# Optimization experiments

Measured on AMD Instinct MI355X. Metric: run time of the kernel, lower is better.

The kernel has to match this reference:

```python
import jax, jax.numpy as jnp
import numpy as np

B = 8192      # env batch
M = 16        # n_machine
HID = 128     # machine_hidden_dim
HEADS = 1
BN_EPS = 1e-5


def _gat(h, gat_W, gat_a):
    # h: (B2, 2, HID); gat_W: (HID, HEADS*HID); gat_a: (HEADS, 2*HID, 1)
    B2 = h.shape[0]
    Wh = (h @ gat_W).reshape(B2, 2, HEADS, HID).transpose(0, 2, 1, 3)  # (B2,H,2,hid)
    src = jnp.einsum('bhnf,hfo->bhno', Wh, gat_a[:, :HID, :])   # (B2,H,2,1)
    tgt = jnp.einsum('bhnf,hfo->bhno', Wh, gat_a[:, HID:, :])   # (B2,H,2,1)
    e = jax.nn.leaky_relu(src + jnp.swapaxes(tgt, -1, -2), negative_slope=0.2)  # (B2,H,2,2)
    # static adjacency: row0 attends to both nodes, row1 only to itself (2->1 directed)
    adj = jnp.array([[1.0, 1.0], [0.0, 1.0]], dtype=e.dtype)
    e = jnp.where(adj > 0, e, jnp.asarray(-9e15, e.dtype))
    att = jax.nn.softmax(e, axis=-1)
    h_prime = att @ Wh                 # (B2,H,2,hid)
    return h_prime.mean(axis=1)        # concat=False -> mean over heads -> (B2,2,hid)


def setup_inputs() -> dict:
    key = jax.random.key(0)
    ks = jax.random.split(key, 24)
    s = 0.05
    inp = {
        'machine_fea_1': jax.random.normal(ks[0], (B, M, 6), jnp.float32),
        'machine_fea_2': jax.random.normal(ks[1], (B, M, 8), jnp.float32),
        'h_pooled_o': jax.random.normal(ks[2], (B, HID), jnp.float32),
        'machine_mask': jnp.zeros((B, 1, M), dtype=bool),
        # params (Linear weights stored as (in, out); original Linears have bias=False for feature projections)
        'W1': jax.random.normal(ks[3], (6, HID), jnp.float32) * s,
        'W2': jax.random.normal(ks[4], (8, HID), jnp.float32) * s,
        'gat_W': jax.random.normal(ks[5], (HID, HEADS * HID), jnp.float32) * s,
        'gat_a': jax.random.normal(ks[6], (HEADS, 2 * HID, 1), jnp.float32) * s,
        'bn_gamma': jnp.ones((HID,), jnp.float32),
        'bn_beta': jnp.zeros((HID,), jnp.float32),
        # MLPActor: 3 layers, in=3*HID, hidden=HID, out=1 (tanh hidden, linear out)
        'Wa1': jax.random.normal(ks[7], (3 * HID, HID), jnp.float32) * s,
        'ba1': jnp.zeros((HID,), jnp.float32),
        'Wa2': jax.random.normal(ks[8], (HID, HID), jnp.float32) * s,
        'ba2': jnp.zeros((HID,), jnp.float32),
        'Wa3': jax.random.normal(ks[9], (HID, 1), jnp.float32) * s,
        'ba3': jnp.zeros((1,), jnp.float32),
        # MLPCritic: 3 layers, in=HID, hidden=HID, out=2
        'Wc1': jax.random.normal(ks[10], (HID, HID), jnp.float32) * s,
        'bc1': jnp.zeros((HID,), jnp.float32),
        'Wc2': jax.random.normal(ks[11], (HID, HID), jnp.float32) * s,
        'bc2': jnp.zeros((HID,), jnp.float32),
        'Wc3': jax.random.normal(ks[12], (HID, 2), jnp.float32) * s,
        'bc3': jnp.zeros((2,), jnp.float32),
    }
    return inp


def reference(machine_fea_1, machine_fea_2, h_pooled_o, machine_mask,
              W1, W2, gat_W, gat_a, bn_gamma, bn_beta,
              Wa1, ba1, Wa2, ba2, Wa3, ba3,
              Wc1, bc1, Wc2, bc2, Wc3, bc3):
    m_fea1 = machine_fea_1 @ W1                       # (B,M,HID)
    m_fea2 = machine_fea_2 @ W2                       # (B,M,HID)
    # pair the two projections per machine node: (B*M, 2, HID)
    h12 = jnp.stack([m_fea1.reshape(-1, HID), m_fea2.reshape(-1, HID)], axis=1)
    g = jax.nn.elu(_gat(h12, gat_W, gat_a))
    g = jax.nn.elu(_gat(g, gat_W, gat_a))
    g = _gat(g, gat_W, gat_a)
    # NOTE: h_machine_feas is computed but unused downstream in the original forward (ablation)
    h_machine_feas = g.mean(axis=-2).reshape(-1, M, HID)
    # BatchNorm1d in training mode over flattened (B*M, HID)
    flat = m_fea1.reshape(-1, HID)
    mu = flat.mean(axis=0)
    var = flat.var(axis=0)  # biased, as torch BN uses for normalization
    h_m_nodes = (((flat - mu) / jnp.sqrt(var + BN_EPS)) * bn_gamma + bn_beta).reshape(-1, M, HID)
    h_pooled = h_m_nodes.mean(axis=1)                 # (B,HID)
    concat = jnp.concatenate([
        h_m_nodes,
        jnp.broadcast_to(h_pooled[:, None, :], h_m_nodes.shape),
        jnp.broadcast_to(h_pooled_o[:, None, :], h_m_nodes.shape),
    ], axis=-1)                                       # (B,M,3*HID)
    x = jnp.tanh(concat @ Wa1 + ba1)
    x = jnp.tanh(x @ Wa2 + ba2)
    mch_scores = (x @ Wa3 + ba3).squeeze(-1) * 10.0   # (B,M)
    mask = machine_mask.squeeze(1)
    mch_scores = jnp.where(mask, -jnp.inf, mch_scores)
    mch_prob = jax.nn.softmax(mch_scores, axis=-1)
    v = jnp.tanh(h_pooled @ Wc1 + bc1)
    v = jnp.tanh(v @ Wc2 + bc2)
    machine_v = v @ Wc3 + bc3                         # (B,2)
    return (mch_prob, h_pooled, machine_v)
```

## Files before the change

kernel.cpp:

```cpp
#include <hip/hip_runtime.h>
#include <hip/hip_bf16.h>
#include <math.h>

#define HID    128
#define BATCH  8192
#define NM     16
#define NROWS  (BATCH * NM)
#define BN_EPS 1e-5f

#define S1_BLOCKS   256
#define S1_ROWS     (NROWS / S1_BLOCKS)
#define PREP_BLOCKS 32
#define TOT_BLOCKS  (S1_BLOCKS + PREP_BLOCKS)

#define WS_PART  0
#define WS_SCALE 8192
#define WS_SHIFT 8320
#define WS_M1    8448
#define WS_SV    9216
#define WS_N1    9344
#define WS_CV    10112
#define WS_BW    10240

#define O1 ((size_t)BATCH * NM)
#define O2 (O1 + (size_t)BATCH * HID)

#define G    4
#define ROWS (G * NM)
#define LDH  136
#define ZLD  136
#define LDV  132
#define HLD  24

typedef __attribute__((ext_vector_type(8))) short short8_t;
typedef __attribute__((ext_vector_type(4))) float f32x4;

#define MFMA16(a, b, c) __builtin_amdgcn_mfma_f32_16x16x32_bf16(a, b, c, 0, 0, 0)

__device__ __forceinline__ unsigned short f2bf(float x) {
    __hip_bfloat16 h = __float2bfloat16(x);
    return *reinterpret_cast<unsigned short*>(&h);
}
__device__ __forceinline__ float bf2f(unsigned short u) {
    __hip_bfloat16 h = *reinterpret_cast<__hip_bfloat16*>(&u);
    return __bfloat162float(h);
}
__device__ __forceinline__ float ftanh(float x) {
    float e = __expf(2.0f * x);
    return 1.0f - 2.0f / (e + 1.0f);
}

__global__ __launch_bounds__(512) void stats_prep_kernel(
    const float* __restrict__ fea1,
    const float* __restrict__ Wa1, const float* __restrict__ Wa2,
    const float* __restrict__ Wc2,
    float* __restrict__ ws, unsigned short* __restrict__ wbt)
{
    const int tid = threadIdx.x;
    const int blk = blockIdx.x;

    if (blk >= S1_BLOCKS) {
        const int idx = (blk - S1_BLOCKS) * 512 + tid;
        const int k = idx >> 7, c = idx & 127;
        wbt[c * 128 + k]         = f2bf(Wa1[idx]);
        wbt[16384 + c * 128 + k] = f2bf(Wa2[idx]);
        wbt[32768 + c * 128 + k] = f2bf(Wa1[32768 + idx]);
        wbt[49152 + c * 128 + k] = f2bf(Wc2[idx]);
        return;
    }

    __shared__ float feaS[S1_ROWS * 6];
    __shared__ float redM[8 * 27];

    const float* src = fea1 + (size_t)blk * (S1_ROWS * 6);
    for (int i = tid; i < S1_ROWS * 6; i += 512) feaS[i] = src[i];
    __syncthreads();

    float f[6];
    #pragma unroll
    for (int j = 0; j < 6; ++j) f[j] = feaS[tid * 6 + j];

    float acc[27];
    #pragma unroll
    for (int j = 0; j < 6; ++j) acc[j] = f[j];
    {
        int idx = 6;
        #pragma unroll
        for (int j = 0; j < 6; ++j)
            #pragma unroll
            for (int k = j; k < 6; ++k) acc[idx++] = f[j] * f[k];
    }
    #pragma unroll
    for (int j = 0; j < 27; ++j) {
        acc[j] += __shfl_xor(acc[j], 1);
        acc[j] += __shfl_xor(acc[j], 2);
        acc[j] += __shfl_xor(acc[j], 4);
        acc[j] += __shfl_xor(acc[j], 8);
        acc[j] += __shfl_xor(acc[j], 16);
        acc[j] += __shfl_xor(acc[j], 32);
    }
    const int wv = tid >> 6;
    if ((tid & 63) == 0) {
        #pragma unroll
        for (int j = 0; j < 27; ++j) redM[wv * 27 + j] = acc[j];
    }
    __syncthreads();
    if (tid < 27) {
        float s = 0.f;
        #pragma unroll
        for (int w2 = 0; w2 < 8; ++w2) s += redM[w2 * 27 + tid];
        ws[WS_PART + blk * 32 + tid] = s;
    }
}

__global__ __launch_bounds__(512) void finalize_kernel(
    const float* __restrict__ W1,  const float* __restrict__ Wa1,
    const float* __restrict__ Wc1, const float* __restrict__ bc1,
    const float* __restrict__ gamma, const float* __restrict__ beta,
    float* __restrict__ ws, unsigned short* __restrict__ wbt)
{
    __shared__ double momS[27];
    __shared__ float scS2[HID], shS[HID];
    __shared__ float w1sS[6 * HID];
    __shared__ float partS[4 * 7 * HID];

    const int tid = threadIdx.x;
    const int blk = blockIdx.x;

    {
        const int j = tid >> 4;
        const int l = tid & 15;
        double s = 0.0;
        if (j < 27)
            for (int p = l; p < S1_BLOCKS; p += 16)
                s += (double)ws[WS_PART + p * 32 + j];
        s += __shfl_xor(s, 1);
        s += __shfl_xor(s, 2);
        s += __shfl_xor(s, 4);
        s += __shfl_xor(s, 8);
        if (j < 27 && l == 0) momS[j] = s;
    }
    __syncthreads();

    if (tid < 128) {
        float wv[6];
        #pragma unroll
        for (int j = 0; j < 6; ++j) wv[j] = W1[j * HID + tid];
        double sum = 0.0, ssq = 0.0;
        #pragma unroll
        for (int j = 0; j < 6; ++j) sum += (double)wv[j] * momS[j];
        {
            int idx = 6;
            #pragma unroll
            for (int j = 0; j < 6; ++j)
                #pragma unroll
                for (int k = j; k < 6; ++k) {
                    double t = (double)wv[j] * (double)wv[k] * momS[idx++];
                    ssq += (j == k) ? t : 2.0 * t;
                }
        }
        const double inv = 1.0 / (double)NROWS;
        double mu  = sum * inv;
        double var = ssq * inv - mu * mu;
        float sc = gamma[tid] * rsqrtf((float)var + BN_EPS);
        float sh = beta[tid] - (float)mu * sc;
        scS2[tid] = sc;
        shS[tid]  = sh;
        if (blk == 0) {
            ws[WS_SCALE + tid] = sc;
            ws[WS_SHIFT + tid] = sh;
        }
    }
    __syncthreads();
    for (int i = tid; i < 6 * HID; i += 512)
        w1sS[i] = W1[i] * scS2[i & 127];
    __syncthreads();

    if (blk == 2) {
        for (int idx = tid; idx < HID * 32; idx += 512) {
            const int col = idx >> 5, k = idx & 31;
            unsigned short v = 0;
            int kr = -1; bool lo = false;
            if (k < 6)                    kr = k;
            else if (k >= 8  && k < 14)   kr = k - 8;
            else if (k >= 16 && k < 22) { kr = k - 16; lo = true; }
            if (kr >= 0) {
                const float wv = w1sS[kr * HID + col];
                const unsigned short hi = f2bf(wv);
                v = lo ? f2bf(wv - bf2f(hi)) : hi;
            }
            wbt[65536 + col * 32 + k] = v;
        }
        return;
    }

    {
        const float* st = (blk == 0) ? (Wa1 + 16384) : Wc1;
        const int cc = tid & 127;
        const int kq = tid >> 7;
        float a[7] = {0.f, 0.f, 0.f, 0.f, 0.f, 0.f, 0.f};
        for (int k = kq * 32; k < kq * 32 + 32; ++k) {
            const float sv = st[k * 128 + cc];
            #pragma unroll
            for (int j = 0; j < 6; ++j)
                a[j] += w1sS[j * HID + k] * sv;
            a[6] += shS[k] * sv;
        }
        #pragma unroll
        for (int j = 0; j < 7; ++j)
            partS[(kq * 7 + j) * HID + cc] = a[j];
    }
    __syncthreads();
    if (tid < 128) {
        #pragma unroll
        for (int j = 0; j < 7; ++j) {
            const float v = partS[(0 * 7 + j) * HID + tid]
                          + partS[(1 * 7 + j) * HID + tid]
                          + partS[(2 * 7 + j) * HID + tid]
                          + partS[(3 * 7 + j) * HID + tid];
            if (blk == 0) {
                if (j < 6) ws[WS_M1 + j * HID + tid] = v;
                else       ws[WS_SV + tid] = v;
            } else {
                if (j < 6) ws[WS_N1 + j * HID + tid] = v;
                else       ws[WS_CV + tid] = v + bc1[tid];
            }
        }
    }
}

__global__ __launch_bounds__(256, 4) void main_kernel(
    const float* __restrict__ fea1, const float* __restrict__ hpo,
    const unsigned char* __restrict__ mask,
    const float* __restrict__ W1,
    const float* __restrict__ ba1, const float* __restrict__ ba2,
    const float* __restrict__ Wa3, const float* __restrict__ ba3,
    const float* __restrict__ bc2,
    const float* __restrict__ Wc3, const float* __restrict__ bc3,
    const float* __restrict__ ws, const unsigned short* __restrict__ wbt,
    float* __restrict__ out)
{
    __shared__ __align__(16) unsigned short hmS[ROWS * LDH];
    __shared__ __align__(16) unsigned short x1S[ROWS * LDH];
    __shared__ __align__(16) unsigned short zS[G * ZLD];
    __shared__ __align__(16) unsigned short v1bS[4 * LDV];
    __shared__ __align__(16) unsigned short v2bS[4 * LDV];
    __shared__ float scS[4 * ROWS];
    __shared__ float fmS[4][8];

    float* feaS = (float*)x1S;
    unsigned short* feaHL = x1S + 768;

    const int tid = threadIdx.x;
    const int b0  = blockIdx.x * G;

    const int w    = tid >> 6;
    const int lane = tid & 63;
    const int lr   = lane & 15;
    const int lg   = lane >> 4;
    const int n0   = 2 * w;

    const unsigned short* wbt1  = wbt;
    const unsigned short* wbt2  = wbt + 16384;
    const unsigned short* wbtB  = wbt + 32768;
    const unsigned short* wbtC2 = wbt + 49152;
    const unsigned short* wbtW1 = wbt + 65536;

    for (int i = tid; i < ROWS * 6; i += 256) {
        const float x = fea1[(size_t)b0 * (NM * 6) + i];
        feaS[i] = x;
        const int r = i / 6, j = i - r * 6;
        const unsigned short hx = f2bf(x);
        const unsigned short lx = f2bf(x - bf2f(hx));
        feaHL[r * HLD + j]     = hx;
        feaHL[r * HLD + 8 + j] = lx;
    }
    if (tid < 64) {
        feaHL[tid * HLD + 6]  = 0;
        feaHL[tid * HLD + 7]  = 0;
        feaHL[tid * HLD + 14] = 0;
        feaHL[tid * HLD + 15] = 0;
    } else if (tid < 80) {
        feaHL[64 * HLD + (tid - 64)] = 0;
    }
    for (int i = tid; i < G * HID; i += 256) {
        const int g = i >> 7, cc = i & 127;
        zS[g * ZLD + cc] = f2bf(hpo[(size_t)b0 * HID + i]);
    }

    short8_t bW[2];
    #pragma unroll
    for (int t = 0; t < 2; ++t)
        bW[t] = *(const short8_t*)(wbtW1 + ((n0 + t) * 16 + lr) * 32 + lg * 8);
    short8_t b1f[2][4];
    #pragma unroll
    for (int t = 0; t < 2; ++t) {
        const unsigned short* br = wbt1 + ((n0 + t) * 16 + lr) * 128 + lg * 8;
        #pragma unroll
        for (int kk = 0; kk < 4; ++kk) b1f[t][kk] = *(const short8_t*)(br + kk * 32);
    }
    const float sh0 = ws[WS_SHIFT + n0 * 16 + lr];
    const float sh1 = ws[WS_SHIFT + (n0 + 1) * 16 + lr];
    __syncthreads();

    const int hloff = (lg == 1) ? 8 : 0;
    #pragma unroll
    for (int g = 0; g < 4; ++g) {
        const int row = (lg == 3) ? 64 : (g * 16 + lr);
        short8_t af = *(const short8_t*)(feaHL + row * HLD + hloff);

        #pragma unroll
        for (int t = 0; t < 2; ++t) {
            const float sh = t ? sh1 : sh0;
            f32x4 acc = {sh, sh, sh, sh};
            acc = MFMA16(af, bW[t], acc);
            #pragma unroll
            for (int i = 0; i < 4; ++i)
                hmS[(g * 16 + lg * 4 + i) * LDH + (n0 + t) * 16 + lr] = f2bf(acc[i]);
        }
    }
    if (tid < 24) {
        const int g = tid / 6, j = tid % 6;
        float s = 0.f;
        for (int m = 0; m < NM; ++m) s += feaS[(g * 16 + m) * 6 + j];
        fmS[g][j] = s * (1.0f / NM);
    }
    __syncthreads();

    f32x4 accB[2];
    {
        short8_t bBf[2][4];
        #pragma unroll
        for (int t = 0; t < 2; ++t) {
            const unsigned short* br = wbtB + ((n0 + t) * 16 + lr) * 128 + lg * 8;
            #pragma unroll
            for (int kk = 0; kk < 4; ++kk) bBf[t][kk] = *(const short8_t*)(br + kk * 32);
        }
        short8_t za[4];
        const unsigned short* zr = zS + (lr & 3) * ZLD + lg * 8;
        #pragma unroll
        for (int kk = 0; kk < 4; ++kk) za[kk] = *(const short8_t*)(zr + kk * 32);

        float fm[4][6];
        #pragma unroll
        for (int g = 0; g < 4; ++g)
            #pragma unroll
            for (int j = 0; j < 6; ++j) fm[g][j] = fmS[g][j];

        #pragma unroll
        for (int t = 0; t < 2; ++t) {
            const int col = (n0 + t) * 16 + lr;
            const float bias = ba1[col] + ws[WS_SV + col];
            float b_[4];
            #pragma unroll
            for (int g = 0; g < 4; ++g) {
                float a = bias;
                #pragma unroll
                for (int j = 0; j < 6; ++j) a += fm[g][j] * ws[WS_M1 + j * HID + col];
                b_[g] = a;
            }
            f32x4 acc = {b_[0], b_[1], b_[2], b_[3]};
            acc = MFMA16(za[0], bBf[t][0], acc);
            acc = MFMA16(za[1], bBf[t][1], acc);
            acc = MFMA16(za[2], bBf[t][2], acc);
            acc = MFMA16(za[3], bBf[t][3], acc);
            accB[t] = acc;
        }

        #pragma unroll
        for (int t = 0; t < 2; ++t) {
            const int col = (n0 + t) * 16 + lr;
            float a = ws[WS_CV + col];
            #pragma unroll
            for (int j = 0; j < 6; ++j) a += fm[lg][j] * ws[WS_N1 + j * HID + col];
            v1bS[lg * LDV + col] = f2bf(ftanh(a));
        }

        #pragma unroll
        for (int t = 0; t < 2; ++t) {
            const int col = (n0 + t) * 16 + lr;
            float a = 0.f;
            #pragma unroll
            for (int j = 0; j < 6; ++j) a += fm[lg][j] * W1[j * HID + col];
            a = a * ws[WS_SCALE + col] + ws[WS_SHIFT + col];
            out[O1 + (size_t)(b0 + lg) * HID + col] = a;
        }
    }

    short8_t b2f[2][4];
    #pragma unroll
    for (int t = 0; t < 2; ++t) {
        const unsigned short* br = wbt2 + ((n0 + t) * 16 + lr) * 128 + lg * 8;
        #pragma unroll
        for (int kk = 0; kk < 4; ++kk) b2f[t][kk] = *(const short8_t*)(br + kk * 32);
    }

    #pragma unroll
    for (int g = 0; g < 4; ++g) {
        short8_t ha[4];
        const unsigned short* ar = hmS + (g * 16 + lr) * LDH + lg * 8;
        #pragma unroll
        for (int kk = 0; kk < 4; ++kk) ha[kk] = *(const short8_t*)(ar + kk * 32);
        #pragma unroll
        for (int t = 0; t < 2; ++t) {
            const float bz = accB[t][g];
            f32x4 acc = {bz, bz, bz, bz};
            acc = MFMA16(ha[0], b1f[t][0], acc);
            acc = MFMA16(ha[1], b1f[t][1], acc);
            acc = MFMA16(ha[2], b1f[t][2], acc);
            acc = MFMA16(ha[3], b1f[t][3], acc);
            #pragma unroll
            for (int i = 0; i < 4; ++i)
                x1S[(g * 16 + lg * 4 + i) * LDH + (n0 + t) * 16 + lr] = f2bf(ftanh(acc[i]));
        }
    }
    __syncthreads();

    {
        short8_t va[4];
        const unsigned short* vr = v1bS + (lr & 3) * LDV + lg * 8;
        #pragma unroll
        for (int kk = 0; kk < 4; ++kk) va[kk] = *(const short8_t*)(vr + kk * 32);
        #pragma unroll
        for (int t = 0; t < 2; ++t) {
            const int n = n0 + t;
            const unsigned short* br = wbtC2 + (n * 16 + lr) * 128 + lg * 8;
            const float bi = bc2[n * 16 + lr];
            f32x4 acc = {bi, bi, bi, bi};
            acc = MFMA16(va[0], *(const short8_t*)(br),      acc);
            acc = MFMA16(va[1], *(const short8_t*)(br + 32), acc);
            acc = MFMA16(va[2], *(const short8_t*)(br + 64), acc);
            acc = MFMA16(va[3], *(const short8_t*)(br + 96), acc);
            if (lg == 0) {
                #pragma unroll
                for (int i = 0; i < 4; ++i)
                    v2bS[i * LDV + n * 16 + lr] = f2bf(ftanh(acc[i]));
            }
        }

        float p[4][4];
        #pragma unroll
        for (int g = 0; g < 4; ++g)
            #pragma unroll
            for (int i = 0; i < 4; ++i) p[g][i] = 0.f;

        const float wv0 = Wa3[n0 * 16 + lr];
        const float wv1 = Wa3[(n0 + 1) * 16 + lr];
        const float bi0 = ba2[n0 * 16 + lr];
        const float bi1 = ba2[(n0 + 1) * 16 + lr];
        #pragma unroll
        for (int g = 0; g < 4; ++g) {
            short8_t ha[4];
            const unsigned short* ar = x1S + (g * 16 + lr) * LDH + lg * 8;
            #pragma unroll
            for (int kk = 0; kk < 4; ++kk) ha[kk] = *(const short8_t*)(ar + kk * 32);
            #pragma unroll
            for (int t = 0; t < 2; ++t) {
                const float bi = t ? bi1 : bi0;
                f32x4 acc = {bi, bi, bi, bi};
                acc = MFMA16(ha[0], b2f[t][0], acc);
                acc = MFMA16(ha[1], b2f[t][1], acc);
                acc = MFMA16(ha[2], b2f[t][2], acc);
                acc = MFMA16(ha[3], b2f[t][3], acc);
                const float wv = t ? wv1 : wv0;
                #pragma unroll
                for (int i = 0; i < 4; ++i)
                    p[g][i] += ftanh(acc[i]) * wv;
            }
        }
        #pragma unroll
        for (int g = 0; g < 4; ++g) {
            #pragma unroll
            for (int i = 0; i < 4; ++i) {
                float v = p[g][i];
                v += __shfl_xor(v, 1);
                v += __shfl_xor(v, 2);
                v += __shfl_xor(v, 4);
                v += __shfl_xor(v, 8);
                if (lr == 0) scS[w * ROWS + g * 16 + lg * 4 + i] = v;
            }
        }
    }
    __syncthreads();

    {
        const int g = w;
        float s = scS[0 * ROWS + g * 16 + lr] + scS[1 * ROWS + g * 16 + lr]
                + scS[2 * ROWS + g * 16 + lr] + scS[3 * ROWS + g * 16 + lr];
        s = (s + ba3[0]) * 10.0f;
        if (mask[(size_t)(b0 + g) * NM + lr]) s = -INFINITY;
        float mx = s;
        mx = fmaxf(mx, __shfl_xor(mx, 1));
        mx = fmaxf(mx, __shfl_xor(mx, 2));
        mx = fmaxf(mx, __shfl_xor(mx, 4));
        mx = fmaxf(mx, __shfl_xor(mx, 8));
        float e = __expf(s - mx);
        float sum = e;
        sum += __shfl_xor(sum, 1);
        sum += __shfl_xor(sum, 2);
        sum += __shfl_xor(sum, 4);
        sum += __shfl_xor(sum, 8);
        if (lane < NM)
            out[(size_t)(b0 + g) * NM + lr] = e / sum;
    }

    {
        const int g = w;
        const int k2 = lane * 2;
        float v0 = bf2f(v2bS[g * LDV + k2]);
        float v1 = bf2f(v2bS[g * LDV + k2 + 1]);
        float4 wc = *(const float4*)(Wc3 + k2 * 2);
        float p0 = v0 * wc.x + v1 * wc.z;
        float p1 = v0 * wc.y + v1 * wc.w;
        p0 += __shfl_xor(p0, 1);  p1 += __shfl_xor(p1, 1);
        p0 += __shfl_xor(p0, 2);  p1 += __shfl_xor(p1, 2);
        p0 += __shfl_xor(p0, 4);  p1 += __shfl_xor(p1, 4);
        p0 += __shfl_xor(p0, 8);  p1 += __shfl_xor(p1, 8);
        p0 += __shfl_xor(p0, 16); p1 += __shfl_xor(p1, 16);
        p0 += __shfl_xor(p0, 32); p1 += __shfl_xor(p1, 32);
        if (lane == 0) {
            out[O2 + (size_t)(b0 + g) * 2 + 0] = p0 + bc3[0];
            out[O2 + (size_t)(b0 + g) * 2 + 1] = p1 + bc3[1];
        }
    }
}

extern "C" void kernel_launch(void* const* d_in, const int* in_sizes, int n_in,
                              void* d_out, int out_size, void* d_ws, size_t ws_size,
                              hipStream_t stream)
{
    const float* fea1  = (const float*)d_in[0];
    const float* hpo   = (const float*)d_in[2];
    const unsigned char* mask = (const unsigned char*)d_in[3];
    const float* W1    = (const float*)d_in[4];
    const float* gamma = (const float*)d_in[8];
    const float* beta  = (const float*)d_in[9];
    const float* Wa1   = (const float*)d_in[10];
    const float* ba1   = (const float*)d_in[11];
    const float* Wa2   = (const float*)d_in[12];
    const float* ba2   = (const float*)d_in[13];
    const float* Wa3   = (const float*)d_in[14];
    const float* ba3   = (const float*)d_in[15];
    const float* Wc1   = (const float*)d_in[16];
    const float* bc1   = (const float*)d_in[17];
    const float* Wc2   = (const float*)d_in[18];
    const float* bc2   = (const float*)d_in[19];
    const float* Wc3   = (const float*)d_in[20];
    const float* bc3   = (const float*)d_in[21];

    float* ws = (float*)d_ws;
    unsigned short* wbt = (unsigned short*)(ws + WS_BW);
    float* out = (float*)d_out;

    stats_prep_kernel<<<TOT_BLOCKS, 512, 0, stream>>>(
        fea1, Wa1, Wa2, Wc2, ws, wbt);
    finalize_kernel<<<3, 512, 0, stream>>>(
        W1, Wa1, Wc1, bc1, gamma, beta, ws, wbt);
    main_kernel<<<BATCH / G, 256, 0, stream>>>(
        fea1, hpo, mask, W1, ba1, ba2, Wa3, ba3,
        bc2, Wc3, bc3, ws, wbt, out);
}
```

Baseline: 67.62 us.

## Double batch tile per block and give each wave one 16-column slice

The main kernel now handles 8 batch elements per block with 512 threads (8 waves) instead of 4 elements with 4 waves. Each wave owns one 16-column output slice instead of two, so it holds half as many weight fragments in registers, and each weight fragment is reused across 8 row groups. The z-projection MFMA outputs are shared between lane groups with cross-lane shuffles, and the score reduction now sums over 8 per-wave partials. This halves the grid size and doubles LDS use per block, which may lower occupancy or leave fewer blocks to balance across CUs.

```diff
diff --git a/kernel.cpp b/kernel.cpp
--- a/kernel.cpp
+++ b/kernel.cpp
@@ -25,7 +25,7 @@
 #define O1 ((size_t)BATCH * NM)
 #define O2 (O1 + (size_t)BATCH * HID)
 
-#define G    4
+#define G    8
 #define ROWS (G * NM)
 #define LDH  136
 #define ZLD  136
@@ -229,7 +229,7 @@
     }
 }
 
-__global__ __launch_bounds__(256, 4) void main_kernel(
+__global__ __launch_bounds__(512, 4) void main_kernel(
     const float* __restrict__ fea1, const float* __restrict__ hpo,
     const unsigned char* __restrict__ mask,
     const float* __restrict__ W1,
@@ -243,13 +243,13 @@
     __shared__ __align__(16) unsigned short hmS[ROWS * LDH];
     __shared__ __align__(16) unsigned short x1S[ROWS * LDH];
     __shared__ __align__(16) unsigned short zS[G * ZLD];
-    __shared__ __align__(16) unsigned short v1bS[4 * LDV];
-    __shared__ __align__(16) unsigned short v2bS[4 * LDV];
-    __shared__ float scS[4 * ROWS];
-    __shared__ float fmS[4][8];
+    __shared__ __align__(16) unsigned short v1bS[G * LDV];
+    __shared__ __align__(16) unsigned short v2bS[G * LDV];
+    __shared__ float scS[8 * ROWS];
+    __shared__ float fmS[G][8];
 
     float* feaS = (float*)x1S;
-    unsigned short* feaHL = x1S + 768;
+    unsigned short* feaHL = x1S + 1536;
 
     const int tid = threadIdx.x;
     const int b0  = blockIdx.x * G;
@@ -258,7 +258,7 @@
     const int lane = tid & 63;
     const int lr   = lane & 15;
     const int lg   = lane >> 4;
-    const int n0   = 2 * w;
+    const int col  = w * 16 + lr;
 
     const unsigned short* wbt1  = wbt;
     const unsigned short* wbt2  = wbt + 16384;
@@ -266,7 +266,7 @@
     const unsigned short* wbtC2 = wbt + 49152;
     const unsigned short* wbtW1 = wbt + 65536;
 
-    for (int i = tid; i < ROWS * 6; i += 256) {
+    for (int i = tid; i < ROWS * 6; i += 512) {
         const float x = fea1[(size_t)b0 * (NM * 6) + i];
         feaS[i] = x;
         const int r = i / 6, j = i - r * 6;
@@ -275,51 +275,41 @@
         feaHL[r * HLD + j]     = hx;
         feaHL[r * HLD + 8 + j] = lx;
     }
-    if (tid < 64) {
+    if (tid < ROWS) {
         feaHL[tid * HLD + 6]  = 0;
         feaHL[tid * HLD + 7]  = 0;
         feaHL[tid * HLD + 14] = 0;
         feaHL[tid * HLD + 15] = 0;
-    } else if (tid < 80) {
-        feaHL[64 * HLD + (tid - 64)] = 0;
-    }
-    for (int i = tid; i < G * HID; i += 256) {
+    } else if (tid < ROWS + 16) {
+        feaHL[ROWS * HLD + (tid - ROWS)] = 0;
+    }
+    for (int i = tid; i < G * HID; i += 512) {
         const int g = i >> 7, cc = i & 127;
         zS[g * ZLD + cc] = f2bf(hpo[(size_t)b0 * HID + i]);
     }
 
-    short8_t bW[2];
-    #pragma unroll
-    for (int t = 0; t < 2; ++t)
-        bW[t] = *(const short8_t*)(wbtW1 + ((n0 + t) * 16 + lr) * 32 + lg * 8);
-    short8_t b1f[2][4];
-    #pragma unroll
-    for (int t = 0; t < 2; ++t) {
-        const unsigned short* br = wbt1 + ((n0 + t) * 16 + lr) * 128 + lg * 8;
-        #pragma unroll
-        for (int kk = 0; kk < 4; ++kk) b1f[t][kk] = *(const short8_t*)(br + kk * 32);
-    }
-    const float sh0 = ws[WS_SHIFT + n0 * 16 + lr];
-    const float sh1 = ws[WS_SHIFT + (n0 + 1) * 16 + lr];
+    short8_t bW = *(const short8_t*)(wbtW1 + col * 32 + lg * 8);
+    short8_t b1f[4];
+    {
+        const unsigned short* br = wbt1 + col * 128 + lg * 8;
+        #pragma unroll
+        for (int kk = 0; kk < 4; ++kk) b1f[kk] = *(const short8_t*)(br + kk * 32);
+    }
+    const float sh = ws[WS_SHIFT + col];
     __syncthreads();
 
     const int hloff = (lg == 1) ? 8 : 0;
     #pragma unroll
-    for (int g = 0; g < 4; ++g) {
-        const int row = (lg == 3) ? 64 : (g * 16 + lr);
+    for (int g = 0; g < G; ++g) {
+        const int row = (lg == 3) ? ROWS : (g * 16 + lr);
         short8_t af = *(const short8_t*)(feaHL + row * HLD + hloff);
-
-        #pragma unroll
-        for (int t = 0; t < 2; ++t) {
-            const float sh = t ? sh1 : sh0;
-            f32x4 acc = {sh, sh, sh, sh};
-            acc = MFMA16(af, bW[t], acc);
-            #pragma unroll
-            for (int i = 0; i < 4; ++i)
-                hmS[(g * 16 + lg * 4 + i) * LDH + (n0 + t) * 16 + lr] = f2bf(acc[i]);
-        }
-    }
-    if (tid < 24) {
+        f32x4 acc = {sh, sh, sh, sh};
+        acc = MFMA16(af, bW, acc);
+        #pragma unroll
+        for (int i = 0; i < 4; ++i)
+            hmS[(g * 16 + lg * 4 + i) * LDH + col] = f2bf(acc[i]);
+    }
+    if (tid < G * 6) {
         const int g = tid / 6, j = tid % 6;
         float s = 0.f;
         for (int m = 0; m < NM; ++m) s += feaS[(g * 16 + m) * 6 + j];
@@ -327,152 +317,124 @@
     }
     __syncthreads();
 
-    f32x4 accB[2];
-    {
-        short8_t bBf[2][4];
-        #pragma unroll
-        for (int t = 0; t < 2; ++t) {
-            const unsigned short* br = wbtB + ((n0 + t) * 16 + lr) * 128 + lg * 8;
-            #pragma unroll
-            for (int kk = 0; kk < 4; ++kk) bBf[t][kk] = *(const short8_t*)(br + kk * 32);
-        }
+    f32x4 accB, accBo;
+    {
         short8_t za[4];
-        const unsigned short* zr = zS + (lr & 3) * ZLD + lg * 8;
+        const unsigned short* zr = zS + (lr & 7) * ZLD + lg * 8;
         #pragma unroll
         for (int kk = 0; kk < 4; ++kk) za[kk] = *(const short8_t*)(zr + kk * 32);
 
-        float fm[4][6];
-        #pragma unroll
-        for (int g = 0; g < 4; ++g)
-            #pragma unroll
-            for (int j = 0; j < 6; ++j) fm[g][j] = fmS[g][j];
-
-        #pragma unroll
-        for (int t = 0; t < 2; ++t) {
-            const int col = (n0 + t) * 16 + lr;
+        {
+            const unsigned short* br = wbtB + col * 128 + lg * 8;
+            short8_t bB0 = *(const short8_t*)(br);
+            short8_t bB1 = *(const short8_t*)(br + 32);
+            short8_t bB2 = *(const short8_t*)(br + 64);
+            short8_t bB3 = *(const short8_t*)(br + 96);
             const float bias = ba1[col] + ws[WS_SV + col];
+            const int gbase = (lg & 1) ? 4 : 0;
             float b_[4];
             #pragma unroll
-            for (int g = 0; g < 4; ++g) {
+            for (int i = 0; i < 4; ++i) {
                 float a = bias;
                 #pragma unroll
-                for (int j = 0; j < 6; ++j) a += fm[g][j] * ws[WS_M1 + j * HID + col];
-                b_[g] = a;
+                for (int j = 0; j < 6; ++j)
+                    a += fmS[gbase + i][j] * ws[WS_M1 + j * HID + col];
+                b_[i] = a;
             }
             f32x4 acc = {b_[0], b_[1], b_[2], b_[3]};
-            acc = MFMA16(za[0], bBf[t][0], acc);
-            acc = MFMA16(za[1], bBf[t][1], acc);
-            acc = MFMA16(za[2], bBf[t][2], acc);
-            acc = MFMA16(za[3], bBf[t][3], acc);
-            accB[t] = acc;
-        }
-
-        #pragma unroll
-        for (int t = 0; t < 2; ++t) {
-            const int col = (n0 + t) * 16 + lr;
+            acc = MFMA16(za[0], bB0, acc);
+            acc = MFMA16(za[1], bB1, acc);
+            acc = MFMA16(za[2], bB2, acc);
+            acc = MFMA16(za[3], bB3, acc);
+            accB = acc;
+            #pragma unroll
+            for (int i = 0; i < 4; ++i) accBo[i] = __shfl_xor(acc[i], 16);
+        }
+
+        #pragma unroll
+        for (int go = 0; go < 2; ++go) {
+            const int g = lg + 4 * go;
             float a = ws[WS_CV + col];
             #pragma unroll
-            for (int j = 0; j < 6; ++j) a += fm[lg][j] * ws[WS_N1 + j * HID + col];
-            v1bS[lg * LDV + col] = f2bf(ftanh(a));
-        }
-
-        #pragma unroll
-        for (int t = 0; t < 2; ++t) {
-            const int col = (n0 + t) * 16 + lr;
+            for (int j = 0; j < 6; ++j) a += fmS[g][j] * ws[WS_N1 + j * HID + col];
+            v1bS[g * LDV + col] = f2bf(ftanh(a));
+        }
+
+        #pragma unroll
+        for (int go = 0; go < 2; ++go) {
+            const int g = lg + 4 * go;
             float a = 0.f;
             #pragma unroll
-            for (int j = 0; j < 6; ++j) a += fm[lg][j] * W1[j * HID + col];
+            for (int j = 0; j < 6; ++j) a += fmS[g][j] * W1[j * HID + col];
             a = a * ws[WS_SCALE + col] + ws[WS_SHIFT + col];
-            out[O1 + (size_t)(b0 + lg) * HID + col] = a;
-        }
-    }
-
-    short8_t b2f[2][4];
+            out[O1 + (size_t)(b0 + g) * HID + col] = a;
+        }
+    }
+
+    short8_t b2f[4];
+    {
+        const unsigned short* br = wbt2 + col * 128 + lg * 8;
+        #pragma unroll
+        for (int kk = 0; kk < 4; ++kk) b2f[kk] = *(const short8_t*)(br + kk * 32);
+    }
+
     #pragma unroll
-    for (int t = 0; t < 2; ++t) {
-        const unsigned short* br = wbt2 + ((n0 + t) * 16 + lr) * 128 + lg * 8;
-        #pragma unroll
-        for (int kk = 0; kk < 4; ++kk) b2f[t][kk] = *(const short8_t*)(br + kk * 32);
-    }
-
-    #pragma unroll
-    for (int g = 0; g < 4; ++g) {
+    for (int g = 0; g < G; ++g) {
         short8_t ha[4];
         const unsigned short* ar = hmS + (g * 16 + lr) * LDH + lg * 8;
         #pragma unroll
         for (int kk = 0; kk < 4; ++kk) ha[kk] = *(const short8_t*)(ar + kk * 32);
-        #pragma unroll
-        for (int t = 0; t < 2; ++t) {
-            const float bz = accB[t][g];
-            f32x4 acc = {bz, bz, bz, bz};
-            acc = MFMA16(ha[0], b1f[t][0], acc);
-            acc = MFMA16(ha[1], b1f[t][1], acc);
-            acc = MFMA16(ha[2], b1f[t][2], acc);
-            acc = MFMA16(ha[3], b1f[t][3], acc);
-            #pragma unroll
-            for (int i = 0; i < 4; ++i)
-                x1S[(g * 16 + lg * 4 + i) * LDH + (n0 + t) * 16 + lr] = f2bf(ftanh(acc[i]));
-        }
+        const float bz = (g < 4)
+            ? ((lg & 1) ? accBo[g]     : accB[g])
+            : ((lg & 1) ? accB[g - 4]  : accBo[g - 4]);
+        f32x4 acc = {bz, bz, bz, bz};
+        acc = MFMA16(ha[0], b1f[0], acc);
+        acc = MFMA16(ha[1], b1f[1], acc);
+        acc = MFMA16(ha[2], b1f[2], acc);
+        acc = MFMA16(ha[3], b1f[3], acc);
+        #pragma unroll
+        for (int i = 0; i < 4; ++i)
+            x1S[(g * 16 + lg * 4 + i) * LDH + col] = f2bf(ftanh(acc[i]));
     }
     __syncthreads();
 
     {
         short8_t va[4];
-        const unsigned short* vr = v1bS + (lr & 3) * LDV + lg * 8;
+        const unsigned short* vr = v1bS + (lr & 7) * LDV + lg * 8;
         #pragma unroll
         for (int kk = 0; kk < 4; ++kk) va[kk] = *(const short8_t*)(vr + kk * 32);
-        #pragma unroll
-        for (int t = 0; t < 2; ++t) {
-            const int n = n0 + t;
-            const unsigned short* br = wbtC2 + (n * 16 + lr) * 128 + lg * 8;
-            const float bi = bc2[n * 16 + lr];
+        {
+            const unsigned short* br = wbtC2 + col * 128 + lg * 8;
+            const float bi = bc2[col];
             f32x4 acc = {bi, bi, bi, bi};
             acc = MFMA16(va[0], *(const short8_t*)(br),      acc);
             acc = MFMA16(va[1], *(const short8_t*)(br + 32), acc);
             acc = MFMA16(va[2], *(const short8_t*)(br + 64), acc);
             acc = MFMA16(va[3], *(const short8_t*)(br + 96), acc);
-            if (lg == 0) {
+            if (lg < 2) {
+                const int gb = lg * 4;
                 #pragma unroll
                 for (int i = 0; i < 4; ++i)
-                    v2bS[i * LDV + n * 16 + lr] = f2bf(ftanh(acc[i]));
+                    v2bS[(gb + i) * LDV + col] = f2bf(ftanh(acc[i]));
             }
         }
 
-        float p[4][4];
-        #pragma unroll
-        for (int g = 0; g < 4; ++g)
-            #pragma unroll
-            for (int i = 0; i < 4; ++i) p[g][i] = 0.f;
-
-        const float wv0 = Wa3[n0 * 16 + lr];
-        const float wv1 = Wa3[(n0 + 1) * 16 + lr];
-        const float bi0 = ba2[n0 * 16 + lr];
-        const float bi1 = ba2[(n0 + 1) * 16 + lr];
-        #pragma unroll
-        for (int g = 0; g < 4; ++g) {
+        const float wv = Wa3[col];
+        const float bi = ba2[col];
+        #pragma unroll
+        for (int g = 0; g < G; ++g) {
             short8_t ha[4];
             const unsigned short* ar = x1S + (g * 16 + lr) * LDH + lg * 8;
             #pragma unroll
             for (int kk = 0; kk < 4; ++kk) ha[kk] = *(const short8_t*)(ar + kk * 32);
-            #pragma unroll
-            for (int t = 0; t < 2; ++t) {
-                const float bi = t ? bi1 : bi0;
-                f32x4 acc = {bi, bi, bi, bi};
-                acc = MFMA16(ha[0], b2f[t][0], acc);
-                acc = MFMA16(ha[1], b2f[t][1], acc);
-                acc = MFMA16(ha[2], b2f[t][2], acc);
-                acc = MFMA16(ha[3], b2f[t][3], acc);
-                const float wv = t ? wv1 : wv0;
-                #pragma unroll
-                for (int i = 0; i < 4; ++i)
-                    p[g][i] += ftanh(acc[i]) * wv;
-            }
-        }
-        #pragma unroll
-        for (int g = 0; g < 4; ++g) {
+            f32x4 acc = {bi, bi, bi, bi};
+            acc = MFMA16(ha[0], b2f[0], acc);
+            acc = MFMA16(ha[1], b2f[1], acc);
+            acc = MFMA16(ha[2], b2f[2], acc);
+            acc = MFMA16(ha[3], b2f[3], acc);
             #pragma unroll
             for (int i = 0; i < 4; ++i) {
-                float v = p[g][i];
+                float v = ftanh(acc[i]) * wv;
                 v += __shfl_xor(v, 1);
                 v += __shfl_xor(v, 2);
                 v += __shfl_xor(v, 4);
@@ -485,8 +447,10 @@
 
     {
         const int g = w;
-        float s = scS[0 * ROWS + g * 16 + lr] + scS[1 * ROWS + g * 16 + lr]
-                + scS[2 * ROWS + g * 16 + lr] + scS[3 * ROWS + g * 16 + lr];
+        float s = 0.f;
+        #pragma unroll
+        for (int w2 = 0; w2 < 8; ++w2)
+            s += scS[w2 * ROWS + g * 16 + lr];
         s = (s + ba3[0]) * 10.0f;
         if (mask[(size_t)(b0 + g) * NM + lr]) s = -INFINITY;
         float mx = s;
@@ -556,7 +520,7 @@
         fea1, Wa1, Wa2, Wc2, ws, wbt);
     finalize_kernel<<<3, 512, 0, stream>>>(
         W1, Wa1, Wc1, bc1, gamma, beta, ws, wbt);
-    main_kernel<<<BATCH / G, 256, 0, stream>>>(
+    main_kernel<<<BATCH / G, 512, 0, stream>>>(
         fea1, hpo, mask, W1, ba1, ba2, Wa3, ba3,
         bc2, Wc3, bc3, ws, wbt, out);
 }
```

After: 63.00 us, median of 2. 1.07x faster.
